# Optimization experiments

Measured on AMD Instinct MI355X. Metric: run time of the kernel, lower is better.

Reference implementation:

```python
import jax, jax.numpy as jnp
import numpy as np

# Faithful JAX reference for MVLiftingModule.lift_2D_to_3D with lifting_method='mean'.
# Torch semantics: for each batch, view, and part p in [1, parts_nb[b]] (in order),
# scatter-write the (weighted softmax) pixel prediction into each point that any
# Since each pixel's predicted part is unique (argmax), the winning pixel per point
# is the one maximizing key = pred_class * H*W + flat_pixel_index. We compute that
# deterministically via scatter-max, then gather features and voint-mean over views.

def setup_inputs() -> dict:
    key = jax.random.key(0)
    k1, k2, k3, k4, k5 = jax.random.split(key, 5)
    B, N, V, C, H, W = 4, 2048, 12, 50, 128, 128
    points = jax.random.normal(k1, (B, N, 3), dtype=jnp.float32)
    predictions_2d = jax.random.normal(k2, (B, V, C, H, W), dtype=jnp.float32)
    # -1 marks background pixels (no point), as in pytorch3d pix_to_face
    rendered_pix_to_point = jax.random.randint(k3, (B, V, 1, H, W), -1, N, dtype=jnp.int32)
    views_weights = jax.random.uniform(k4, (B, V, 1, 1, 1), dtype=jnp.float32)
    parts_nb = jax.random.randint(k5, (B,), 1, 7, dtype=jnp.int32)
    return {"points": points, "predictions_2d": predictions_2d,
            "rendered_pix_to_point": rendered_pix_to_point,
            "views_weights": views_weights, "parts_nb": parts_nb}


def reference(points, predictions_2d, rendered_pix_to_point, views_weights, parts_nb):
    B, N, _ = points.shape
    _, V, C, H, W = predictions_2d.shape
    P = H * W

    p2p = rendered_pix_to_point[:, :, 0]            # (B,V,H,W)
    valid = p2p != -1                                # pix_to_face_mask
    idx = jnp.where(valid, p2p % N, 0)               # invalid pixels -> point 0 (as in torch)

    probs = jax.nn.softmax(predictions_2d, axis=2)   # softmax over classes
    pred_max = jnp.argmax(probs, axis=2).astype(jnp.int32)   # (B,V,H,W)
    feats = (views_weights * probs).reshape(B, V, C, P)       # weighted predictions

    # pixel participates iff valid and its predicted part in [1, parts_nb[b]]
    mask_pix = valid & (pred_max >= 1) & (pred_max <= parts_nb[:, None, None, None])
    mask_pix = mask_pix.reshape(B, V, P)
    idx_f = idx.reshape(B, V, P)

    pix = jnp.arange(P, dtype=jnp.int32)
    kkey = pred_max.reshape(B, V, P) * P + pix
    kkey = jnp.where(mask_pix, kkey, -1)

    bi = jnp.arange(B)[:, None, None]
    vi = jnp.arange(V)[None, :, None]
    winner = jnp.full((B, V, N), -1, dtype=jnp.int32).at[bi, vi, idx_f].max(kkey)

    voints_mask = (winner >= 0)                      # (B,V,N)
    win_pix = jnp.where(voints_mask, winner % P, 0)  # winning pixel per point/view

    # gather weighted features at winning pixel: (B,V,C,N)
    point_feats = jnp.take_along_axis(feats, win_pix[:, :, None, :], axis=3)
    m = voints_mask.astype(feats.dtype)
    masked = point_feats * m[:, :, None, :]

    # vointmean: masked mean over views -> (B,C,N)
    denom = jnp.maximum(m.sum(axis=1), 1.0)          # (B,N)
    labels_3d_feats = masked.sum(axis=1) / denom[:, None, :]
    return labels_3d_feats
```

## Files before the change

### kernel.cpp

```cpp
#include <hip/hip_runtime.h>

#define B 4
#define N 2048
#define V 12
#define C 50
#define P 16384
#define PSTRIDE 56

__global__ __launch_bounds__(256, 2) void k1_fused(
    const float* __restrict__ pred,
    const int*   __restrict__ p2p,
    const int*   __restrict__ parts_nb,
    int*         __restrict__ winner,
    float*       __restrict__ pool) {
  int t = blockIdx.x * 256 + threadIdx.x;
  int p  = t & (P - 1);
  int bv = t >> 14;
  int b  = bv / V;

  const float* pp = pred + (size_t)bv * C * P + p;
  float l[C];
  #pragma unroll
  for (int c = 0; c < C; ++c) l[c] = pp[(size_t)c * P];

  float m = l[0];
  int   a = 0;
  #pragma unroll
  for (int c = 1; c < C; ++c) if (l[c] > m) { m = l[c]; a = c; }

  int pt = p2p[(size_t)bv * P + p];
  int pn = parts_nb[b];
  if (pt != -1 && a >= 1 && a <= pn) {
    float s = 0.f;
    float* dst = pool + (size_t)(bv * P + p) * PSTRIDE;
    #pragma unroll
    for (int c = 0; c < C; ++c) { float e = __expf(l[c]); dst[c] = e; s += e; }
    dst[C] = s;
    atomicMax(&winner[bv * N + pt], a * P + p);
  }
}

__global__ __launch_bounds__(256) void k3_reduce(
    const int*   __restrict__ winner,
    const float* __restrict__ pool,
    const float* __restrict__ vw,
    float*       __restrict__ out) {
  int wid  = blockIdx.x * 4 + (threadIdx.x >> 6);
  int lane = threadIdx.x & 63;
  int b = wid >> 11;
  int n = wid & (N - 1);

  float acc = 0.f;
  int cnt = 0;
  #pragma unroll
  for (int v = 0; v < V; ++v) {
    int bv  = b * V + v;
    int key = winner[bv * N + n];
    bool valid = key >= 0;
    int wp = key & (P - 1);
    const float* src = pool + (size_t)(bv * P + wp) * PSTRIDE;
    float e = (valid && lane < C) ? src[lane] : 0.f;
    float s = valid ? src[C] : 1.f;
    float f = valid ? (vw[bv] / s) : 0.f;
    cnt += valid ? 1 : 0;
    acc += e * f;
  }
  if (lane < C)
    out[((size_t)b * C + lane) * N + n] = acc / (float)(cnt > 0 ? cnt : 1);
}

extern "C" void kernel_launch(void* const* d_in, const int* in_sizes, int n_in,
                              void* d_out, int out_size, void* d_ws, size_t ws_size,
                              hipStream_t stream) {
  const float* pred  = (const float*)d_in[1];
  const int*   p2p   = (const int*)d_in[2];
  const float* vw    = (const float*)d_in[3];
  const int*   parts = (const int*)d_in[4];
  float* out = (float*)d_out;

  char* ws = (char*)d_ws;
  int*   winner = (int*)ws;
  float* pool   = (float*)(ws + (size_t)B * V * N * sizeof(int) + 128);

  hipMemsetAsync(winner, 0xFF, (size_t)B * V * N * sizeof(int), stream);

  int nthreads = B * V * P;
  k1_fused<<<nthreads / 256, 256, 0, stream>>>(
      pred, p2p, parts, winner, pool);

  k3_reduce<<<(B * N) / 4, 256, 0, stream>>>(winner, pool, vw, out);
}
```

Baseline: 255.1 us.

## Process two pixels per thread with vector loads and stores, stage reduce output in LDS

The fused kernel now handles two adjacent pixels per thread using float2 loads of logits and int2 loads of point indices. It writes the exp values with float4 stores into a tighter 52-float pool stride, and subtracts the max before exponentiating. The reduce kernel preloads all view keys, skips invalid views with a branch, and stages results in shared memory so the output stores are grouped across the four points of a block. The aim is fewer memory transactions and more memory-level parallelism. The cost is doubled register pressure for the logits array, which could lower occupancy.

Result: no change. 252.0 us (-1.2%).

```diff
diff --git a/kernel.cpp b/kernel.cpp
--- a/kernel.cpp
+++ b/kernel.cpp
@@ -5,7 +5,7 @@
 #define V 12
 #define C 50
 #define P 16384
-#define PSTRIDE 56
+#define PSTRIDE 52
 
 __global__ __launch_bounds__(256, 2) void k1_fused(
     const float* __restrict__ pred,
@@ -13,30 +13,58 @@
     const int*   __restrict__ parts_nb,
     int*         __restrict__ winner,
     float*       __restrict__ pool) {
-  int t = blockIdx.x * 256 + threadIdx.x;
-  int p  = t & (P - 1);
-  int bv = t >> 14;
+  int t  = blockIdx.x * 256 + threadIdx.x;
+  int p2 = t & (P / 2 - 1);
+  int bv = t >> 13;
   int b  = bv / V;
+  int p0 = p2 * 2;
 
-  const float* pp = pred + (size_t)bv * C * P + p;
-  float l[C];
+  const float* pp = pred + (size_t)bv * C * P + p0;
+  float2 l[C];
   #pragma unroll
-  for (int c = 0; c < C; ++c) l[c] = pp[(size_t)c * P];
+  for (int c = 0; c < C; ++c)
+    l[c] = *reinterpret_cast<const float2*>(pp + (size_t)c * P);
 
-  float m = l[0];
-  int   a = 0;
+  float m0 = l[0].x, m1 = l[0].y;
+  int   a0 = 0,      a1 = 0;
   #pragma unroll
-  for (int c = 1; c < C; ++c) if (l[c] > m) { m = l[c]; a = c; }
+  for (int c = 1; c < C; ++c) {
+    if (l[c].x > m0) { m0 = l[c].x; a0 = c; }
+    if (l[c].y > m1) { m1 = l[c].y; a1 = c; }
+  }
 
-  int pt = p2p[(size_t)bv * P + p];
-  int pn = parts_nb[b];
-  if (pt != -1 && a >= 1 && a <= pn) {
+  int2 pt = *reinterpret_cast<const int2*>(p2p + (size_t)bv * P + p0);
+  int  pn = parts_nb[b];
+
+  if (pt.x != -1 && a0 >= 1 && a0 <= pn) {
+    float* dst = pool + (size_t)(bv * P + p0) * PSTRIDE;
     float s = 0.f;
-    float* dst = pool + (size_t)(bv * P + p) * PSTRIDE;
     #pragma unroll
-    for (int c = 0; c < C; ++c) { float e = __expf(l[c]); dst[c] = e; s += e; }
-    dst[C] = s;
-    atomicMax(&winner[bv * N + pt], a * P + p);
+    for (int c = 0; c < 48; c += 4) {
+      float4 v = make_float4(__expf(l[c].x - m0),   __expf(l[c+1].x - m0),
+                             __expf(l[c+2].x - m0), __expf(l[c+3].x - m0));
+      s += (v.x + v.y) + (v.z + v.w);
+      *reinterpret_cast<float4*>(dst + c) = v;
+    }
+    float e48 = __expf(l[48].x - m0), e49 = __expf(l[49].x - m0);
+    s += e48 + e49;
+    *reinterpret_cast<float4*>(dst + 48) = make_float4(e48, e49, s, 0.f);
+    atomicMax(&winner[bv * N + pt.x], a0 * P + p0);
+  }
+  if (pt.y != -1 && a1 >= 1 && a1 <= pn) {
+    float* dst = pool + (size_t)(bv * P + p0 + 1) * PSTRIDE;
+    float s = 0.f;
+    #pragma unroll
+    for (int c = 0; c < 48; c += 4) {
+      float4 v = make_float4(__expf(l[c].y - m1),   __expf(l[c+1].y - m1),
+                             __expf(l[c+2].y - m1), __expf(l[c+3].y - m1));
+      s += (v.x + v.y) + (v.z + v.w);
+      *reinterpret_cast<float4*>(dst + c) = v;
+    }
+    float e48 = __expf(l[48].y - m1), e49 = __expf(l[49].y - m1);
+    s += e48 + e49;
+    *reinterpret_cast<float4*>(dst + 48) = make_float4(e48, e49, s, 0.f);
+    atomicMax(&winner[bv * N + pt.y], a1 * P + p0 + 1);
   }
 }
 
@@ -45,28 +73,42 @@
     const float* __restrict__ pool,
     const float* __restrict__ vw,
     float*       __restrict__ out) {
-  int wid  = blockIdx.x * 4 + (threadIdx.x >> 6);
+  __shared__ float sm[4][52];
+  int w    = threadIdx.x >> 6;
   int lane = threadIdx.x & 63;
+  int wid  = blockIdx.x * 4 + w;
   int b = wid >> 11;
   int n = wid & (N - 1);
+
+  int keys[V];
+  #pragma unroll
+  for (int v = 0; v < V; ++v)
+    keys[v] = winner[(b * V + v) * N + n];
 
   float acc = 0.f;
   int cnt = 0;
   #pragma unroll
   for (int v = 0; v < V; ++v) {
-    int bv  = b * V + v;
-    int key = winner[bv * N + n];
-    bool valid = key >= 0;
-    int wp = key & (P - 1);
-    const float* src = pool + (size_t)(bv * P + wp) * PSTRIDE;
-    float e = (valid && lane < C) ? src[lane] : 0.f;
-    float s = valid ? src[C] : 1.f;
-    float f = valid ? (vw[bv] / s) : 0.f;
-    cnt += valid ? 1 : 0;
-    acc += e * f;
+    int key = keys[v];
+    if (key >= 0) {
+      int bv = b * V + v;
+      const float* src = pool + (size_t)(bv * P + (key & (P - 1))) * PSTRIDE;
+      float e = (lane < C) ? src[lane] : 0.f;
+      float f = vw[bv] / src[C];
+      acc += e * f;
+      ++cnt;
+    }
   }
-  if (lane < C)
-    out[((size_t)b * C + lane) * N + n] = acc / (float)(cnt > 0 ? cnt : 1);
+  if (lane < C) sm[w][lane] = acc / (float)(cnt > 0 ? cnt : 1);
+  __syncthreads();
+
+  int tid = threadIdx.x;
+  if (tid < 4 * C) {
+    int c = tid >> 2, j = tid & 3;
+    int b_blk = (blockIdx.x * 4) >> 11;
+    int n_blk = (blockIdx.x * 4) & (N - 1);
+    out[((size_t)b_blk * C + c) * N + n_blk + j] = sm[j][c];
+  }
 }
 
 extern "C" void kernel_launch(void* const* d_in, const int* in_sizes, int n_in,
@@ -84,7 +126,7 @@
 
   hipMemsetAsync(winner, 0xFF, (size_t)B * V * N * sizeof(int), stream);
 
-  int nthreads = B * V * P;
+  int nthreads = B * V * P / 2;
   k1_fused<<<nthreads / 256, 256, 0, stream>>>(
       pred, p2p, parts, winner, pool);
 
```
